# Performance work log

Hardware: AMD Instinct MI355X
Metric: run time of the kernel (lower is better)

Reference implementation:

```python
import jax, jax.numpy as jnp
import numpy as np


def setup_inputs() -> dict:
    key = jax.random.key(0)
    k1, k2 = jax.random.split(key)
    B, F_in, N, F_out = 4, 64, 8192, 64
    x = jax.random.normal(k1, (B, F_in, N), dtype=jnp.float32)
    stdv = 1.0 / np.sqrt(F_out)
    weight = jax.random.uniform(k2, (F_in, F_out), dtype=jnp.float32, minval=-stdv, maxval=stdv)
    return {"x": x, "weight": weight}


def reference(x, weight):
    # x: [B, F_in, N], weight: [F_in, F_out]
    x_t = jnp.transpose(x, (0, 2, 1))              # [B, N, F_in]
    support = jnp.einsum('bnf,fo->bno', x_t, weight)  # [B, N, F_out]
    adj = jnp.einsum('bnf,bfm->bnm', x_t, x)       # [B, N, N]
    adj = jax.nn.softmax(adj, axis=2)
    out = jnp.einsum('bnm,bmo->bno', adj, support) # [B, N, F_out]
    return jnp.transpose(out, (0, 2, 1))           # [B, F_out, N]
```

## Files before the change

kernel.cpp:

```cpp
#include <hip/hip_runtime.h>

#define BATCH 4
#define NPTS  8192
#define FDIM  64
#define BK    64
#define NT    (NPTS / BK)

typedef _Float16 half_t;
typedef half_t half8  __attribute__((ext_vector_type(8)));
typedef float  f32x4  __attribute__((ext_vector_type(4)));
typedef float  f32x16 __attribute__((ext_vector_type(16)));
typedef unsigned uint4v __attribute__((ext_vector_type(4)));
typedef unsigned uint2v __attribute__((ext_vector_type(2)));

__device__ inline unsigned pkrtz(float a, float b) {
    return __builtin_bit_cast(unsigned, __builtin_amdgcn_cvt_pkrtz(a, b));
}

__device__ inline uint2v plswap(unsigned a, unsigned b) {
#if __has_builtin(__builtin_amdgcn_permlane32_swap)
    return __builtin_amdgcn_permlane32_swap(a, b, false, false);
#else
    asm volatile("s_nop 1\n\tv_permlane32_swap_b32 %0, %1\n\ts_nop 1"
                 : "+v"(a), "+v"(b));
    uint2v r; r[0] = a; r[1] = b; return r;
#endif
}

__global__ __launch_bounds__(128) void prep_kernel(
    const float* __restrict__ x, const float* __restrict__ w,
    half_t* __restrict__ q, half_t* __restrict__ vt, float* __restrict__ nrm)
{
    __shared__ float wl[FDIM * FDIM];
    int t = threadIdx.x;
    #pragma unroll
    for (int i = 0; i < (FDIM * FDIM) / 128; ++i)
        wl[i * 128 + t] = w[i * 128 + t];
    __syncthreads();

    int gid = blockIdx.x * 128 + t;
    int b = gid >> 13;
    int n = gid & (NPTS - 1);
    const float* xb = x + (size_t)b * FDIM * NPTS + n;

    float acc[FDIM];
    #pragma unroll
    for (int o = 0; o < FDIM; ++o) acc[o] = 0.0f;
    float nr = 0.0f;

    half8* qrow = (half8*)(q + (size_t)gid * FDIM);
    #pragma unroll
    for (int f8 = 0; f8 < 8; ++f8) {
        half8 h;
        #pragma unroll
        for (int j = 0; j < 8; ++j) {
            int f = f8 * 8 + j;
            float xv = xb[(size_t)f * NPTS];
            nr += xv * xv;
            h[j] = (half_t)xv;
            const f32x4* wr = (const f32x4*)&wl[f * FDIM];
            #pragma unroll
            for (int o4 = 0; o4 < FDIM / 4; ++o4) {
                f32x4 wv = wr[o4];
                acc[o4*4+0] += xv * wv[0];
                acc[o4*4+1] += xv * wv[1];
                acc[o4*4+2] += xv * wv[2];
                acc[o4*4+3] += xv * wv[3];
            }
        }
        qrow[f8] = h;
    }
    nrm[gid] = nr * 1.44269504f;
    half_t* vb = vt + (size_t)b * FDIM * NPTS + n;
    #pragma unroll
    for (int o = 0; o < FDIM; ++o)
        vb[(size_t)o * NPTS] = (half_t)acc[o];
}

template<int SPLIT>
__global__ __launch_bounds__(256, 2) void flash_kernel(
    const half_t* __restrict__ qk, const half_t* __restrict__ vt,
    const float* __restrict__ nrm, float* __restrict__ out,
    float* __restrict__ part, float* __restrict__ lbuf)
{
    constexpr int TPS   = NT / SPLIT;
    constexpr int TOTAL = BATCH * SPLIT * (NPTS / 256);

    __shared__ half_t kl[2][BK * FDIM];
    __shared__ half_t vl[2][FDIM * BK];

    int t    = threadIdx.x;
    int lane = t & 63;
    int w    = t >> 6;
    int l31  = lane & 31;
    int hi   = lane >> 5;

    int blk0 = blockIdx.x;
    int blk  = (blk0 & 7) * (TOTAL / 8) + (blk0 >> 3);
    int qc   = blk & 31;
    int rest = blk >> 5;
    int s    = rest & (SPLIT - 1);
    int b    = rest / SPLIT;
    int qw   = qc * 256 + w * 64;

    const half_t* kg = qk + (size_t)b * NPTS * FDIM;
    const half_t* vg = vt + (size_t)b * FDIM * NPTS;

    half8 qf[2][4];
    #pragma unroll
    for (int qt = 0; qt < 2; ++qt)
        #pragma unroll
        for (int c = 0; c < 4; ++c) {
            qf[qt][c] = *(const half8*)(kg + (size_t)(qw + qt*32 + l31) * FDIM + c*16 + hi*8);
            qf[qt][c] = qf[qt][c] * (half_t)1.44269504f;
        }

    float m2[2];
    #pragma unroll
    for (int qt = 0; qt < 2; ++qt)
        m2[qt] = nrm[(size_t)b * NPTS + qw + qt*32 + l31];

    int r0 = t >> 3, g0 = t & 7;
    int r1 = r0 + 32;
    int li0 = r0 * FDIM + ((g0 ^ (r0 & 7)) * 8);
    int li1 = r1 * FDIM + ((g0 ^ (r1 & 7)) * 8);

    int kb0 = s * TPS * BK;
    half8 s0 = *(const half8*)(kg + (size_t)(kb0 + r0) * FDIM + g0*8);
    half8 s1 = *(const half8*)(kg + (size_t)(kb0 + r1) * FDIM + g0*8);
    half8 s2 = *(const half8*)(vg + (size_t)r0 * NPTS + kb0 + g0*8);
    half8 s3 = *(const half8*)(vg + (size_t)r1 * NPTS + kb0 + g0*8);

    f32x16 O[2][2];
    #pragma unroll
    for (int ot = 0; ot < 2; ++ot)
        #pragma unroll
        for (int qt = 0; qt < 2; ++qt)
            #pragma unroll
            for (int r = 0; r < 16; ++r) O[ot][qt][r] = 0.0f;
    float lsum[2] = {0.0f, 0.0f};

    for (int tt = 0; tt < TPS; ++tt) {
        half_t* klb = kl[tt & 1];
        half_t* vlb = vl[tt & 1];
        *(half8*)(klb + li0) = s0;
        *(half8*)(klb + li1) = s1;
        *(half8*)(vlb + li0) = s2;
        *(half8*)(vlb + li1) = s3;
        if (tt + 1 < TPS) {
            int kb = kb0 + (tt + 1) * BK;
            s0 = *(const half8*)(kg + (size_t)(kb + r0) * FDIM + g0*8);
            s1 = *(const half8*)(kg + (size_t)(kb + r1) * FDIM + g0*8);
            s2 = *(const half8*)(vg + (size_t)r0 * NPTS + kb + g0*8);
            s3 = *(const half8*)(vg + (size_t)r1 * NPTS + kb + g0*8);
        }
        __syncthreads();

        f32x16 S[2][2];
        #pragma unroll
        for (int ct = 0; ct < 2; ++ct)
            #pragma unroll
            for (int r = 0; r < 16; ++r) { S[ct][0][r] = -m2[0]; S[ct][1][r] = -m2[1]; }

        #pragma unroll
        for (int ct = 0; ct < 2; ++ct) {
            int krow = ct * 32 + l31;
            #pragma unroll
            for (int c = 0; c < 4; ++c) {
                half8 kf = *(const half8*)(klb + krow * FDIM + (((2*c + hi) ^ (krow & 7)) * 8));
                S[ct][0] = __builtin_amdgcn_mfma_f32_32x32x16_f16(kf, qf[0][c], S[ct][0], 0, 0, 0);
                S[ct][1] = __builtin_amdgcn_mfma_f32_32x32x16_f16(kf, qf[1][c], S[ct][1], 0, 0, 0);
            }
        }

        unsigned pkv[2][2][8];
        #pragma unroll
        for (int ct = 0; ct < 2; ++ct)
            #pragma unroll
            for (int qt = 0; qt < 2; ++qt) {
                float p[16];
                #pragma unroll
                for (int r = 0; r < 16; ++r) {
                    p[r] = __builtin_amdgcn_exp2f(S[ct][qt][r]);
                    lsum[qt] += p[r];
                }
                #pragma unroll
                for (int rr = 0; rr < 8; ++rr)
                    pkv[ct][qt][rr] = pkrtz(p[2*rr], p[2*rr+1]);
            }

        #pragma unroll
        for (int kt = 0; kt < 4; ++kt) {
            const int ct = kt >> 1, i0 = (kt & 1) * 4;
            half8 pb[2];
            #pragma unroll
            for (int qt = 0; qt < 2; ++qt) {
                uint2v r02 = plswap(pkv[ct][qt][i0+0], pkv[ct][qt][i0+2]);
                uint2v r13 = plswap(pkv[ct][qt][i0+1], pkv[ct][qt][i0+3]);
                uint4v uu; uu[0] = r02[0]; uu[1] = r13[0]; uu[2] = r02[1]; uu[3] = r13[1];
                pb[qt] = __builtin_bit_cast(half8, uu);
            }
            #pragma unroll
            for (int ot = 0; ot < 2; ++ot) {
                int vrow = ot * 32 + l31;
                half8 vf = *(const half8*)(vlb + vrow * FDIM + (((2*kt + hi) ^ (vrow & 7)) * 8));
                O[ot][0] = __builtin_amdgcn_mfma_f32_32x32x16_f16(vf, pb[0], O[ot][0], 0, 0, 0);
                O[ot][1] = __builtin_amdgcn_mfma_f32_32x32x16_f16(vf, pb[1], O[ot][1], 0, 0, 0);
            }
        }
    }

    lsum[0] += __shfl_xor(lsum[0], 32);
    lsum[1] += __shfl_xor(lsum[1], 32);

    if constexpr (SPLIT == 1) {
        float inv[2] = {1.0f / lsum[0], 1.0f / lsum[1]};
        size_t ob = (size_t)b * FDIM * NPTS;
        #pragma unroll
        for (int qt = 0; qt < 2; ++qt)
            #pragma unroll
            for (int ot = 0; ot < 2; ++ot)
                #pragma unroll
                for (int r = 0; r < 16; ++r) {
                    int o = ot*32 + (r & 3) + 8*(r >> 2) + 4*hi;
                    out[ob + (size_t)o * NPTS + qw + qt*32 + l31] = O[ot][qt][r] * inv[qt];
                }
    } else {
        float* pbase = part + (size_t)(s * BATCH + b) * FDIM * NPTS;
        #pragma unroll
        for (int qt = 0; qt < 2; ++qt)
            #pragma unroll
            for (int ot = 0; ot < 2; ++ot)
                #pragma unroll
                for (int r = 0; r < 16; ++r) {
                    int o = ot*32 + (r & 3) + 8*(r >> 2) + 4*hi;
                    pbase[(size_t)o * NPTS + qw + qt*32 + l31] = O[ot][qt][r];
                }
        if (hi == 0) {
            float* lb = lbuf + (size_t)(s * BATCH + b) * NPTS + qw;
            lb[l31]      = lsum[0];
            lb[32 + l31] = lsum[1];
        }
    }
}

template<int SPLIT>
__global__ __launch_bounds__(256) void combine_kernel(
    const float* __restrict__ part, const float* __restrict__ lbuf,
    float* __restrict__ out)
{
    int gid  = blockIdx.x * 256 + threadIdx.x;
    int q4   = gid & (NPTS/4 - 1);
    int rest = gid >> 11;
    int b    = rest >> 6;
    size_t ro = (size_t)rest * NPTS + (size_t)q4 * 4;

    f32x4 acc = {0,0,0,0}, ls = {0,0,0,0};
    #pragma unroll
    for (int s = 0; s < SPLIT; ++s) {
        acc += *(const f32x4*)(part + (size_t)s * BATCH * FDIM * NPTS + ro);
        ls  += *(const f32x4*)(lbuf + (size_t)(s * BATCH + b) * NPTS + (size_t)q4 * 4);
    }
    *(f32x4*)(out + ro) = acc / ls;
}

extern "C" void kernel_launch(void* const* d_in, const int* in_sizes, int n_in,
                              void* d_out, int out_size, void* d_ws, size_t ws_size,
                              hipStream_t stream) {
    (void)in_sizes; (void)n_in; (void)out_size;
    const float* x = (const float*)d_in[0];
    const float* w = (const float*)d_in[1];
    float* out = (float*)d_out;

    const size_t qelems = (size_t)BATCH * NPTS * FDIM;
    half_t* q  = (half_t*)d_ws;
    half_t* vt = q + qelems;
    float* nrm = (float*)((char*)d_ws + 2 * qelems * sizeof(half_t));
    float* part = nrm + (size_t)BATCH * NPTS;

    const size_t part_elems = (size_t)BATCH * FDIM * NPTS;
    const size_t l_elems    = (size_t)BATCH * NPTS;
    const size_t base_bytes = 2 * qelems * sizeof(half_t) + (size_t)BATCH * NPTS * sizeof(float);
    const size_t per_split  = (part_elems + l_elems) * sizeof(float);

    int split = 1;
    if (ws_size >= base_bytes + 4 * per_split)      split = 4;
    else if (ws_size >= base_bytes + 2 * per_split) split = 2;
    float* lbuf = part + (size_t)split * part_elems;

    prep_kernel<<<(BATCH * NPTS) / 128, 128, 0, stream>>>(x, w, q, vt, nrm);

    if (split == 4) {
        flash_kernel<4><<<BATCH * 4 * (NPTS / 256), 256, 0, stream>>>(q, vt, nrm, out, part, lbuf);
        combine_kernel<4><<<(BATCH * FDIM * NPTS) / 4 / 256, 256, 0, stream>>>(part, lbuf, out);
    } else if (split == 2) {
        flash_kernel<2><<<BATCH * 2 * (NPTS / 256), 256, 0, stream>>>(q, vt, nrm, out, part, lbuf);
        combine_kernel<2><<<(BATCH * FDIM * NPTS) / 4 / 256, 256, 0, stream>>>(part, lbuf, out);
    } else {
        flash_kernel<1><<<BATCH * 1 * (NPTS / 256), 256, 0, stream>>>(q, vt, nrm, out, nullptr, nullptr);
    }
}
```

Baseline: 100.0 us.

## Use direct global-to-LDS loads, fp16 partials, split-8, and restructured softmax loop

The K/V tile staging moves from register-staged loads and LDS stores to global_load_lds direct transfers issued after the barrier. The S/exp/PV work is restructured per 32-column chunk to lower register pressure, which allows raising the occupancy hint to 3, and s_setprio is placed around the MFMA groups. The row sum is accumulated in packed fp16 adds. Partial outputs are written as fp16, halving combine traffic, which makes an 8-way key split fit in the workspace. This trades some accumulation precision in the partials and row sums for less memory traffic and more parallelism.

```diff
diff --git a/kernel.cpp b/kernel.cpp
--- a/kernel.cpp
+++ b/kernel.cpp
@@ -8,6 +8,7 @@
 
 typedef _Float16 half_t;
 typedef half_t half8  __attribute__((ext_vector_type(8)));
+typedef half_t half2v __attribute__((ext_vector_type(2)));
 typedef float  f32x4  __attribute__((ext_vector_type(4)));
 typedef float  f32x16 __attribute__((ext_vector_type(16)));
 typedef unsigned uint4v __attribute__((ext_vector_type(4)));
@@ -16,15 +17,17 @@
 __device__ inline unsigned pkrtz(float a, float b) {
     return __builtin_bit_cast(unsigned, __builtin_amdgcn_cvt_pkrtz(a, b));
 }
+__device__ inline half2v h2(unsigned u) { return __builtin_bit_cast(half2v, u); }
 
 __device__ inline uint2v plswap(unsigned a, unsigned b) {
-#if __has_builtin(__builtin_amdgcn_permlane32_swap)
     return __builtin_amdgcn_permlane32_swap(a, b, false, false);
-#else
-    asm volatile("s_nop 1\n\tv_permlane32_swap_b32 %0, %1\n\ts_nop 1"
-                 : "+v"(a), "+v"(b));
-    uint2v r; r[0] = a; r[1] = b; return r;
-#endif
+}
+
+typedef __attribute__((address_space(3))) unsigned lds_u32_t;
+typedef __attribute__((address_space(1))) const unsigned glb_u32_t;
+__device__ inline void gload_lds16(const half_t* g, half_t* l) {
+    __builtin_amdgcn_global_load_lds((glb_u32_t*)(const unsigned*)g,
+                                     (lds_u32_t*)(unsigned*)l, 16, 0, 0);
 }
 
 __global__ __launch_bounds__(128) void prep_kernel(
@@ -78,16 +81,16 @@
 }
 
 template<int SPLIT>
-__global__ __launch_bounds__(256, 2) void flash_kernel(
+__global__ __launch_bounds__(256, 3) void flash_kernel(
     const half_t* __restrict__ qk, const half_t* __restrict__ vt,
     const float* __restrict__ nrm, float* __restrict__ out,
-    float* __restrict__ part, float* __restrict__ lbuf)
+    half_t* __restrict__ part, float* __restrict__ lbuf)
 {
     constexpr int TPS   = NT / SPLIT;
     constexpr int TOTAL = BATCH * SPLIT * (NPTS / 256);
 
     __shared__ half_t kl[2][BK * FDIM];
-    __shared__ half_t vl[2][FDIM * BK];
+    __shared__ half_t vl[2][BK * FDIM];
 
     int t    = threadIdx.x;
     int lane = t & 63;
@@ -120,16 +123,23 @@
     for (int qt = 0; qt < 2; ++qt)
         m2[qt] = nrm[(size_t)b * NPTS + qw + qt*32 + l31];
 
-    int r0 = t >> 3, g0 = t & 7;
-    int r1 = r0 + 32;
-    int li0 = r0 * FDIM + ((g0 ^ (r0 & 7)) * 8);
-    int li1 = r1 * FDIM + ((g0 ^ (r1 & 7)) * 8);
-
     int kb0 = s * TPS * BK;
-    half8 s0 = *(const half8*)(kg + (size_t)(kb0 + r0) * FDIM + g0*8);
-    half8 s1 = *(const half8*)(kg + (size_t)(kb0 + r1) * FDIM + g0*8);
-    half8 s2 = *(const half8*)(vg + (size_t)r0 * NPTS + kb0 + g0*8);
-    half8 s3 = *(const half8*)(vg + (size_t)r1 * NPTS + kb0 + g0*8);
+
+    #define STAGE(kb, buf)                                                        \
+    {                                                                             \
+        _Pragma("unroll")                                                         \
+        for (int i = 0; i < 2; ++i) {                                             \
+            int c  = t + i * 256;                                                 \
+            int r  = c >> 3;                                                      \
+            int gg = (c & 7) ^ (r & 7);                                           \
+            half_t* kd = kl[buf] + (size_t)(w * 64 + i * 256) * 8;                \
+            half_t* vd = vl[buf] + (size_t)(w * 64 + i * 256) * 8;                \
+            gload_lds16(kg + (size_t)((kb) + r) * FDIM + gg * 8, kd);             \
+            gload_lds16(vg + (size_t)r * NPTS + (kb) + gg * 8, vd);               \
+        }                                                                         \
+    }
+
+    STAGE(kb0, 0);
 
     f32x16 O[2][2];
     #pragma unroll
@@ -141,74 +151,64 @@
     float lsum[2] = {0.0f, 0.0f};
 
     for (int tt = 0; tt < TPS; ++tt) {
-        half_t* klb = kl[tt & 1];
-        half_t* vlb = vl[tt & 1];
-        *(half8*)(klb + li0) = s0;
-        *(half8*)(klb + li1) = s1;
-        *(half8*)(vlb + li0) = s2;
-        *(half8*)(vlb + li1) = s3;
-        if (tt + 1 < TPS) {
-            int kb = kb0 + (tt + 1) * BK;
-            s0 = *(const half8*)(kg + (size_t)(kb + r0) * FDIM + g0*8);
-            s1 = *(const half8*)(kg + (size_t)(kb + r1) * FDIM + g0*8);
-            s2 = *(const half8*)(vg + (size_t)r0 * NPTS + kb + g0*8);
-            s3 = *(const half8*)(vg + (size_t)r1 * NPTS + kb + g0*8);
-        }
         __syncthreads();
-
-        f32x16 S[2][2];
-        #pragma unroll
-        for (int ct = 0; ct < 2; ++ct)
-            #pragma unroll
-            for (int r = 0; r < 16; ++r) { S[ct][0][r] = -m2[0]; S[ct][1][r] = -m2[1]; }
+        if (tt + 1 < TPS)
+            STAGE(kb0 + (tt + 1) * BK, ((tt + 1) & 1));
+
+        const half_t* klb = kl[tt & 1];
+        const half_t* vlb = vl[tt & 1];
 
         #pragma unroll
         for (int ct = 0; ct < 2; ++ct) {
+            f32x16 S[2];
+            #pragma unroll
+            for (int r = 0; r < 16; ++r) { S[0][r] = -m2[0]; S[1][r] = -m2[1]; }
             int krow = ct * 32 + l31;
+            __builtin_amdgcn_s_setprio(1);
             #pragma unroll
             for (int c = 0; c < 4; ++c) {
                 half8 kf = *(const half8*)(klb + krow * FDIM + (((2*c + hi) ^ (krow & 7)) * 8));
-                S[ct][0] = __builtin_amdgcn_mfma_f32_32x32x16_f16(kf, qf[0][c], S[ct][0], 0, 0, 0);
-                S[ct][1] = __builtin_amdgcn_mfma_f32_32x32x16_f16(kf, qf[1][c], S[ct][1], 0, 0, 0);
+                S[0] = __builtin_amdgcn_mfma_f32_32x32x16_f16(kf, qf[0][c], S[0], 0, 0, 0);
+                S[1] = __builtin_amdgcn_mfma_f32_32x32x16_f16(kf, qf[1][c], S[1], 0, 0, 0);
+            }
+            __builtin_amdgcn_s_setprio(0);
+
+            unsigned pk[2][8];
+            #pragma unroll
+            for (int qt = 0; qt < 2; ++qt) {
+                #pragma unroll
+                for (int rr = 0; rr < 8; ++rr)
+                    pk[qt][rr] = pkrtz(__builtin_amdgcn_exp2f(S[qt][2*rr]),
+                                       __builtin_amdgcn_exp2f(S[qt][2*rr+1]));
+                half2v s2 = ((h2(pk[qt][0]) + h2(pk[qt][1])) + (h2(pk[qt][2]) + h2(pk[qt][3])))
+                          + ((h2(pk[qt][4]) + h2(pk[qt][5])) + (h2(pk[qt][6]) + h2(pk[qt][7])));
+                lsum[qt] += (float)s2[0] + (float)s2[1];
+            }
+
+            #pragma unroll
+            for (int ktl = 0; ktl < 2; ++ktl) {
+                const int kt = ct * 2 + ktl, i0 = ktl * 4;
+                half8 pb[2];
+                #pragma unroll
+                for (int qt = 0; qt < 2; ++qt) {
+                    uint2v r02 = plswap(pk[qt][i0+0], pk[qt][i0+2]);
+                    uint2v r13 = plswap(pk[qt][i0+1], pk[qt][i0+3]);
+                    uint4v uu; uu[0] = r02[0]; uu[1] = r13[0]; uu[2] = r02[1]; uu[3] = r13[1];
+                    pb[qt] = __builtin_bit_cast(half8, uu);
+                }
+                int vrow0 = l31, vrow1 = 32 + l31;
+                half8 vf0 = *(const half8*)(vlb + vrow0 * FDIM + (((2*kt + hi) ^ (vrow0 & 7)) * 8));
+                half8 vf1 = *(const half8*)(vlb + vrow1 * FDIM + (((2*kt + hi) ^ (vrow1 & 7)) * 8));
+                __builtin_amdgcn_s_setprio(1);
+                O[0][0] = __builtin_amdgcn_mfma_f32_32x32x16_f16(vf0, pb[0], O[0][0], 0, 0, 0);
+                O[0][1] = __builtin_amdgcn_mfma_f32_32x32x16_f16(vf0, pb[1], O[0][1], 0, 0, 0);
+                O[1][0] = __builtin_amdgcn_mfma_f32_32x32x16_f16(vf1, pb[0], O[1][0], 0, 0, 0);
+                O[1][1] = __builtin_amdgcn_mfma_f32_32x32x16_f16(vf1, pb[1], O[1][1], 0, 0, 0);
+                __builtin_amdgcn_s_setprio(0);
             }
         }
-
-        unsigned pkv[2][2][8];
-        #pragma unroll
-        for (int ct = 0; ct < 2; ++ct)
-            #pragma unroll
-            for (int qt = 0; qt < 2; ++qt) {
-                float p[16];
-                #pragma unroll
-                for (int r = 0; r < 16; ++r) {
-                    p[r] = __builtin_amdgcn_exp2f(S[ct][qt][r]);
-                    lsum[qt] += p[r];
-                }
-                #pragma unroll
-                for (int rr = 0; rr < 8; ++rr)
-                    pkv[ct][qt][rr] = pkrtz(p[2*rr], p[2*rr+1]);
-            }
-
-        #pragma unroll
-        for (int kt = 0; kt < 4; ++kt) {
-            const int ct = kt >> 1, i0 = (kt & 1) * 4;
-            half8 pb[2];
-            #pragma unroll
-            for (int qt = 0; qt < 2; ++qt) {
-                uint2v r02 = plswap(pkv[ct][qt][i0+0], pkv[ct][qt][i0+2]);
-                uint2v r13 = plswap(pkv[ct][qt][i0+1], pkv[ct][qt][i0+3]);
-                uint4v uu; uu[0] = r02[0]; uu[1] = r13[0]; uu[2] = r02[1]; uu[3] = r13[1];
-                pb[qt] = __builtin_bit_cast(half8, uu);
-            }
-            #pragma unroll
-            for (int ot = 0; ot < 2; ++ot) {
-                int vrow = ot * 32 + l31;
-                half8 vf = *(const half8*)(vlb + vrow * FDIM + (((2*kt + hi) ^ (vrow & 7)) * 8));
-                O[ot][0] = __builtin_amdgcn_mfma_f32_32x32x16_f16(vf, pb[0], O[ot][0], 0, 0, 0);
-                O[ot][1] = __builtin_amdgcn_mfma_f32_32x32x16_f16(vf, pb[1], O[ot][1], 0, 0, 0);
-            }
-        }
-    }
+    }
+    #undef STAGE
 
     lsum[0] += __shfl_xor(lsum[0], 32);
     lsum[1] += __shfl_xor(lsum[1], 32);
@@ -226,7 +226,7 @@
                     out[ob + (size_t)o * NPTS + qw + qt*32 + l31] = O[ot][qt][r] * inv[qt];
                 }
     } else {
-        float* pbase = part + (size_t)(s * BATCH + b) * FDIM * NPTS;
+        half_t* pbase = part + (size_t)(s * BATCH + b) * FDIM * NPTS;
         #pragma unroll
         for (int qt = 0; qt < 2; ++qt)
             #pragma unroll
@@ -234,7 +234,7 @@
                 #pragma unroll
                 for (int r = 0; r < 16; ++r) {
                     int o = ot*32 + (r & 3) + 8*(r >> 2) + 4*hi;
-                    pbase[(size_t)o * NPTS + qw + qt*32 + l31] = O[ot][qt][r];
+                    pbase[(size_t)o * NPTS + qw + qt*32 + l31] = (half_t)O[ot][qt][r];
                 }
         if (hi == 0) {
             float* lb = lbuf + (size_t)(s * BATCH + b) * NPTS + qw;
@@ -246,22 +246,29 @@
 
 template<int SPLIT>
 __global__ __launch_bounds__(256) void combine_kernel(
-    const float* __restrict__ part, const float* __restrict__ lbuf,
+    const half_t* __restrict__ part, const float* __restrict__ lbuf,
     float* __restrict__ out)
 {
     int gid  = blockIdx.x * 256 + threadIdx.x;
-    int q4   = gid & (NPTS/4 - 1);
-    int rest = gid >> 11;
+    int q8   = gid & (NPTS/8 - 1);
+    int rest = gid >> 10;
     int b    = rest >> 6;
-    size_t ro = (size_t)rest * NPTS + (size_t)q4 * 4;
-
-    f32x4 acc = {0,0,0,0}, ls = {0,0,0,0};
+    size_t ro = (size_t)rest * NPTS + (size_t)q8 * 8;
+
+    float acc[8], ls[8];
+    #pragma unroll
+    for (int j = 0; j < 8; ++j) { acc[j] = 0.0f; ls[j] = 0.0f; }
     #pragma unroll
     for (int s = 0; s < SPLIT; ++s) {
-        acc += *(const f32x4*)(part + (size_t)s * BATCH * FDIM * NPTS + ro);
-        ls  += *(const f32x4*)(lbuf + (size_t)(s * BATCH + b) * NPTS + (size_t)q4 * 4);
-    }
-    *(f32x4*)(out + ro) = acc / ls;
+        half8 pv = *(const half8*)(part + (size_t)s * BATCH * FDIM * NPTS + ro);
+        const float* lb = lbuf + (size_t)(s * BATCH + b) * NPTS + (size_t)q8 * 8;
+        #pragma unroll
+        for (int j = 0; j < 8; ++j) { acc[j] += (float)pv[j]; ls[j] += lb[j]; }
+    }
+    #pragma unroll
+    for (int j = 0; j < 8; ++j) acc[j] /= ls[j];
+    *(f32x4*)(out + ro)     = *(f32x4*)&acc[0];
+    *(f32x4*)(out + ro + 4) = *(f32x4*)&acc[4];
 }
 
 extern "C" void kernel_launch(void* const* d_in, const int* in_sizes, int n_in,
@@ -276,26 +283,30 @@
     half_t* q  = (half_t*)d_ws;
     half_t* vt = q + qelems;
     float* nrm = (float*)((char*)d_ws + 2 * qelems * sizeof(half_t));
-    float* part = nrm + (size_t)BATCH * NPTS;
+    half_t* part = (half_t*)(nrm + (size_t)BATCH * NPTS);
 
     const size_t part_elems = (size_t)BATCH * FDIM * NPTS;
     const size_t l_elems    = (size_t)BATCH * NPTS;
     const size_t base_bytes = 2 * qelems * sizeof(half_t) + (size_t)BATCH * NPTS * sizeof(float);
-    const size_t per_split  = (part_elems + l_elems) * sizeof(float);
+    const size_t per_split  = part_elems * sizeof(half_t) + l_elems * sizeof(float);
 
     int split = 1;
-    if (ws_size >= base_bytes + 4 * per_split)      split = 4;
+    if (ws_size >= base_bytes + 8 * per_split)      split = 8;
+    else if (ws_size >= base_bytes + 4 * per_split) split = 4;
     else if (ws_size >= base_bytes + 2 * per_split) split = 2;
-    float* lbuf = part + (size_t)split * part_elems;
+    float* lbuf = (float*)(part + (size_t)split * part_elems);
 
     prep_kernel<<<(BATCH * NPTS) / 128, 128, 0, stream>>>(x, w, q, vt, nrm);
 
-    if (split == 4) {
+    if (split == 8) {
+        flash_kernel<8><<<BATCH * 8 * (NPTS / 256), 256, 0, stream>>>(q, vt, nrm, out, part, lbuf);
+        combine_kernel<8><<<(BATCH * FDIM * NPTS) / 8 / 256, 256, 0, stream>>>(part, lbuf, out);
+    } else if (split == 4) {
         flash_kernel<4><<<BATCH * 4 * (NPTS / 256), 256, 0, stream>>>(q, vt, nrm, out, part, lbuf);
-        combine_kernel<4><<<(BATCH * FDIM * NPTS) / 4 / 256, 256, 0, stream>>>(part, lbuf, out);
+        combine_kernel<4><<<(BATCH * FDIM * NPTS) / 8 / 256, 256, 0, stream>>>(part, lbuf, out);
     } else if (split == 2) {
         flash_kernel<2><<<BATCH * 2 * (NPTS / 256), 256, 0, stream>>>(q, vt, nrm, out, part, lbuf);
-        combine_kernel<2><<<(BATCH * FDIM * NPTS) / 4 / 256, 256, 0, stream>>>(part, lbuf, out);
+        combine_kernel<2><<<(BATCH * FDIM * NPTS) / 8 / 256, 256, 0, stream>>>(part, lbuf, out);
     } else {
         flash_kernel<1><<<BATCH * 1 * (NPTS / 256), 256, 0, stream>>>(q, vt, nrm, out, nullptr, nullptr);
     }
```

Measured after the change: 243.8 us. +143.8%, slower.
